# Kernel optimization log

Hardware: AMD Instinct MI355X
Metric: run time of the kernel (lower is better)

The kernel has to match this reference:

```python
import jax, jax.numpy as jnp
import numpy as np

N, H, IN, E = 4096, 64, 64, 10  # notes, hidden, input feat, edge types


def setup_inputs() -> dict:
    key = jax.random.key(0)
    ks = jax.random.split(key, 7)
    std_a = (2.0 / (H + H)) ** 0.5
    std_b = (2.0 / (IN + H)) ** 0.5
    return {
        "input": jax.random.normal(ks[0], (1, N, IN), jnp.float32),
        "hidden": jax.random.normal(ks[1], (1, N, H), jnp.float32),
        # dense per-edge-type adjacency; scaled by 1/N to keep gate pre-activations O(1)
        "edge_matrix": jax.random.uniform(ks[2], (E, N, N), jnp.float32) / N,
        "ba": jnp.zeros((H,), jnp.float32),
        "wz_wr_wh": jax.random.normal(ks[3], (E, H, 3 * H), jnp.float32) * std_a,
        "uz_ur": jax.random.normal(ks[4], (H, 2 * H), jnp.float32) * std_a,
        "uh": jax.random.normal(ks[5], (H, H), jnp.float32) * std_a,
        "input_wzrh": jax.random.normal(ks[6], (IN, 3 * H), jnp.float32) * std_b,
        "iteration": 10,
    }


def reference(input, hidden, edge_matrix, ba, wz_wr_wh, uz_ur, uh, input_wzrh, iteration):
    B, n, _ = input.shape          # B == 1
    h_dim = uh.shape[0]
    n_type = wz_wr_wh.shape[0]
    edge_T = jnp.swapaxes(edge_matrix, 1, 2)          # [E, N, N]
    inp_wzrh = jnp.matmul(input, input_wzrh)          # [B, N, 3H] (loop-invariant)

    def step(h, _):
        # message aggregation per edge type: [E,N,N] @ [B,N,H] -> [E,N,H]
        act = jnp.matmul(edge_T, h) + ba
        # per-edge-type gate projections: [E,N,H] @ [E,H,3H] -> [E,N,3H]
        act_wzrh = jnp.matmul(act, wz_wr_wh) + inp_wzrh
        wz, wr, wh = jnp.split(act_wzrh, 3, axis=-1)
        uz, ur = jnp.split(jnp.matmul(h, uz_ur), 2, axis=-1)  # [B,N,H] each
        z = jax.nn.sigmoid(wz.sum(0) + uz)
        r = jax.nn.sigmoid(wr.sum(0) + ur)
        h_tilde = jnp.tanh(wh.reshape(B, n_type, n, h_dim).sum(1)
                           + jnp.matmul(r * h, uh))
        return (1.0 - z) * h + z * h_tilde, None

    hidden, _ = jax.lax.scan(step, hidden, None, length=iteration)
    return hidden
```

## Files before the change

### kernel.cpp

```cpp
#include <hip/hip_runtime.h>
#include <hip/hip_bf16.h>


typedef __bf16 bf16;
typedef bf16 bf16x8 __attribute__((ext_vector_type(8)));
typedef float f32x4 __attribute__((ext_vector_type(4)));

static_assert(sizeof(bf16) == 2, "bf16 size");

constexpr int kN = 4096;
constexpr int kH = 64;
constexpr int kE = 10;
constexpr int kIter = 10;

constexpr size_t OFF_EDGET = 0;
constexpr size_t SZ_EDGET  = (size_t)kE * kN * kN * 2;
constexpr size_t OFF_HF32  = OFF_EDGET + SZ_EDGET;
constexpr size_t OFF_HBF   = OFF_HF32 + (size_t)kN * kH * 4;
constexpr size_t OFF_HT    = OFF_HBF + (size_t)kN * kH * 2;
constexpr size_t OFF_S     = OFF_HT + (size_t)kN * kH * 2;
constexpr size_t OFF_SBIAS = OFF_S + (size_t)kN * 192 * 4;
constexpr size_t OFF_WT    = OFF_SBIAS + (size_t)kN * 192 * 4;
constexpr size_t OFF_UZT   = OFF_WT + (size_t)kE * 192 * 64 * 2;
constexpr size_t OFF_UHT   = OFF_UZT + (size_t)128 * 64 * 2;
constexpr size_t WS_NEEDED = OFF_UHT + (size_t)64 * 64 * 2;

__device__ __forceinline__ void async16(const void* g, void* l) {
  __builtin_amdgcn_global_load_lds(
      (const __attribute__((address_space(1))) unsigned int*)g,
      (__attribute__((address_space(3))) unsigned int*)l, 16, 0, 0);
}

__device__ __forceinline__ float sigmoidf_(float x) { return 1.0f / (1.0f + __expf(-x)); }
__device__ __forceinline__ float tanhf_(float x) { return 1.0f - 2.0f / (__expf(2.0f * x) + 1.0f); }


__global__ __launch_bounds__(256) void k_transpose(const float* __restrict__ edge,
                                                   bf16* __restrict__ edgeT) {
  const int e = blockIdx.z;
  const int m0 = blockIdx.y * 64;
  const int n0 = blockIdx.x * 64;
  __shared__ bf16 t[64 * 66];
  const float* src = edge + (size_t)e * kN * kN;
  for (int i = threadIdx.x; i < 4096; i += 256) {
    int m = i >> 6, n = i & 63;
    t[n * 66 + m] = (bf16)src[(size_t)(m0 + m) * kN + n0 + n];
  }
  __syncthreads();
  bf16* dst = edgeT + (size_t)e * kN * kN;
  for (int i = threadIdx.x; i < 4096; i += 256) {
    int n = i >> 6, m = i & 63;
    dst[(size_t)(n0 + n) * kN + m0 + m] = t[n * 66 + m];
  }
}

__global__ __launch_bounds__(256) void k_weights(const float* __restrict__ wzwrwh,
                                                 const float* __restrict__ uz_ur,
                                                 const float* __restrict__ uh,
                                                 bf16* __restrict__ WT_all,
                                                 bf16* __restrict__ uzurT,
                                                 bf16* __restrict__ uhT) {
  int idx = blockIdx.x * 256 + threadIdx.x;
  if (idx < kE * 192 * 64) {
    int e = idx / (192 * 64);
    int rem = idx % (192 * 64);
    int c = rem / 64, hh = rem % 64;
    WT_all[idx] = (bf16)wzwrwh[((size_t)e * 64 + hh) * 192 + c];
  }
  if (idx < 128 * 64) {
    int c = idx / 64, hh = idx % 64;
    uzurT[idx] = (bf16)uz_ur[hh * 128 + c];
  }
  if (idx < 64 * 64) {
    int c = idx / 64, hh = idx % 64;
    uhT[idx] = (bf16)uh[hh * 64 + c];
  }
}

__global__ __launch_bounds__(256) void k_hinit(const float* __restrict__ hidden,
                                               float* __restrict__ hf32,
                                               bf16* __restrict__ hbf,
                                               bf16* __restrict__ hT) {
  int idx = blockIdx.x * 256 + threadIdx.x;
  float x = hidden[idx];
  hf32[idx] = x;
  hbf[idx] = (bf16)x;
  int n = idx >> 6, c = idx & 63;
  hT[(size_t)c * kN + n] = (bf16)x;
}

__global__ __launch_bounds__(256) void k_sbias(const float* __restrict__ input,
                                               const float* __restrict__ input_wzrh,
                                               float* __restrict__ SBias,
                                               float* __restrict__ S) {
  int idx = blockIdx.x * 256 + threadIdx.x;
  int n = idx / 192, c = idx % 192;
  float a = 0.f;
#pragma unroll 8
  for (int k = 0; k < 64; k++) a += input[n * 64 + k] * input_wzrh[k * 192 + c];
  a *= (float)kE;
  SBias[idx] = a;
  S[idx] = a;
}

__global__ __launch_bounds__(256) void k_copy(const float* __restrict__ src, float* __restrict__ dst) {
  int idx = blockIdx.x * 256 + threadIdx.x;
  dst[idx] = src[idx];
}

__global__ __launch_bounds__(256, 3) void kA(const bf16* __restrict__ edgeT,
                                             const bf16* __restrict__ hT,
                                             const bf16* __restrict__ WT_all,
                                             const float* __restrict__ ba,
                                             float* __restrict__ S) {
  const int e = blockIdx.y;
  const int n0 = blockIdx.x * 64;
  const int tid = threadIdx.x;
  const int lane = tid & 63;
  const int w = tid >> 6;
  const int l15 = lane & 15;
  const int q = lane >> 4;

  __shared__ bf16 Alds[64 * 64];
  __shared__ bf16 Blds[64 * 64];
  __shared__ bf16 Wlds[192 * 72];
  __shared__ bf16 actlds[64 * 72];

  {
    const bf16* src = WT_all + (size_t)e * 192 * 64;
    for (int i = tid; i < 192 * 8; i += 256) {
      int row = i >> 3, col = (i & 7) * 8;
      *(int4*)(Wlds + row * 72 + col) = *(const int4*)(src + row * 64 + col);
    }
  }

  f32x4 acc[4] = {};
  const bf16* Abase = edgeT + (size_t)e * kN * kN + (size_t)n0 * kN;

  for (int k0 = 0; k0 < kN; k0 += 64) {
    __syncthreads();
#pragma unroll
    for (int i = 0; i < 2; i++) {
      int c = i * 256 + tid;
      int row = c >> 3;
      int col = ((c & 7) ^ (row & 7)) * 8;
      async16(Abase + (size_t)row * kN + k0 + col, Alds + c * 8);
    }
#pragma unroll
    for (int i = 0; i < 2; i++) {
      int c = i * 256 + tid;
      int row = c >> 3;
      int col = ((c & 7) ^ (row & 7)) * 8;
      async16(hT + (size_t)row * kN + k0 + col, Blds + c * 8);
    }
    __syncthreads();
#pragma unroll
    for (int ks = 0; ks < 2; ks++) {
      const int ar = w * 16 + l15;
      bf16x8 af = *(const bf16x8*)(Alds + ar * 64 + ((ks * 32 + q * 8) ^ ((ar & 7) << 3)));
#pragma unroll
      for (int ct = 0; ct < 4; ct++) {
        const int br = ct * 16 + l15;
        bf16x8 bf = *(const bf16x8*)(Blds + br * 64 + ((ks * 32 + q * 8) ^ ((br & 7) << 3)));
        acc[ct] = __builtin_amdgcn_mfma_f32_16x16x32_bf16(af, bf, acc[ct], 0, 0, 0);
      }
    }
  }

  __syncthreads();
#pragma unroll
  for (int ct = 0; ct < 4; ct++) {
    int col = ct * 16 + l15;
    float bav = ba[col];
#pragma unroll
    for (int r = 0; r < 4; r++) {
      int row = w * 16 + q * 4 + r;
      actlds[row * 72 + col] = (bf16)(acc[ct][r] + bav);
    }
  }
  __syncthreads();

  f32x4 acc2[12] = {};
#pragma unroll
  for (int ks = 0; ks < 2; ks++) {
    bf16x8 af = *(const bf16x8*)(actlds + (w * 16 + l15) * 72 + ks * 32 + q * 8);
#pragma unroll
    for (int ct = 0; ct < 12; ct++) {
      bf16x8 bf = *(const bf16x8*)(Wlds + (ct * 16 + l15) * 72 + ks * 32 + q * 8);
      acc2[ct] = __builtin_amdgcn_mfma_f32_16x16x32_bf16(af, bf, acc2[ct], 0, 0, 0);
    }
  }
#pragma unroll
  for (int ct = 0; ct < 12; ct++) {
    int col = ct * 16 + l15;
#pragma unroll
    for (int r = 0; r < 4; r++) {
      int row = n0 + w * 16 + q * 4 + r;
      unsafeAtomicAdd(&S[(size_t)row * 192 + col], acc2[ct][r]);
    }
  }
}

__global__ __launch_bounds__(256) void kB(float* __restrict__ S,
                                          const float* __restrict__ SBias,
                                          const bf16* __restrict__ hbf,
                                          const float* __restrict__ hf32,
                                          const bf16* __restrict__ uzurT,
                                          const bf16* __restrict__ uhT,
                                          float* __restrict__ hf32_out,
                                          bf16* __restrict__ hbf_out,
                                          bf16* __restrict__ hT_out,
                                          float* __restrict__ dst) {
  const int n0 = blockIdx.x * 64;
  const int tid = threadIdx.x;
  const int lane = tid & 63;
  const int w = tid >> 6;
  const int l15 = lane & 15;
  const int q = lane >> 4;

  __shared__ bf16 hA[64 * 72];
  __shared__ bf16 uzT[128 * 72];
  __shared__ bf16 uhl[64 * 72];
  __shared__ bf16 rhl[64 * 72];

  for (int i = tid; i < 64 * 8; i += 256) {
    int row = i >> 3, col = (i & 7) * 8;
    *(int4*)(hA + row * 72 + col) = *(const int4*)(hbf + (size_t)(n0 + row) * 64 + col);
  }
  for (int i = tid; i < 128 * 8; i += 256) {
    int row = i >> 3, col = (i & 7) * 8;
    *(int4*)(uzT + row * 72 + col) = *(const int4*)(uzurT + (size_t)row * 64 + col);
  }
  for (int i = tid; i < 64 * 8; i += 256) {
    int row = i >> 3, col = (i & 7) * 8;
    *(int4*)(uhl + row * 72 + col) = *(const int4*)(uhT + (size_t)row * 64 + col);
  }
  __syncthreads();

  f32x4 u[8] = {};
#pragma unroll
  for (int ks = 0; ks < 2; ks++) {
    bf16x8 af = *(const bf16x8*)(hA + (w * 16 + l15) * 72 + ks * 32 + q * 8);
#pragma unroll
    for (int ct = 0; ct < 8; ct++) {
      bf16x8 bf = *(const bf16x8*)(uzT + (ct * 16 + l15) * 72 + ks * 32 + q * 8);
      u[ct] = __builtin_amdgcn_mfma_f32_16x16x32_bf16(af, bf, u[ct], 0, 0, 0);
    }
  }

  float zv[4][4], hv[4][4];
#pragma unroll
  for (int ct = 0; ct < 4; ct++) {
    int col = ct * 16 + l15;
#pragma unroll
    for (int r = 0; r < 4; r++) {
      int row = n0 + w * 16 + q * 4 + r;
      float sz = S[(size_t)row * 192 + col];
      float sr = S[(size_t)row * 192 + 64 + col];
      float z = sigmoidf_(sz + u[ct][r]);
      float rr = sigmoidf_(sr + u[4 + ct][r]);
      float h = hf32[(size_t)row * 64 + col];
      zv[ct][r] = z;
      hv[ct][r] = h;
      rhl[(w * 16 + q * 4 + r) * 72 + col] = (bf16)(rr * h);
    }
  }
  __syncthreads();

  f32x4 t[4] = {};
#pragma unroll
  for (int ks = 0; ks < 2; ks++) {
    bf16x8 af = *(const bf16x8*)(rhl + (w * 16 + l15) * 72 + ks * 32 + q * 8);
#pragma unroll
    for (int ct = 0; ct < 4; ct++) {
      bf16x8 bf = *(const bf16x8*)(uhl + (ct * 16 + l15) * 72 + ks * 32 + q * 8);
      t[ct] = __builtin_amdgcn_mfma_f32_16x16x32_bf16(af, bf, t[ct], 0, 0, 0);
    }
  }

  float hn[4][4];
#pragma unroll
  for (int ct = 0; ct < 4; ct++) {
    int col = ct * 16 + l15;
#pragma unroll
    for (int r = 0; r < 4; r++) {
      int row = n0 + w * 16 + q * 4 + r;
      float wh = S[(size_t)row * 192 + 128 + col];
      float htl = tanhf_(wh + t[ct][r]);
      float z = zv[ct][r];
      float v = (1.0f - z) * hv[ct][r] + z * htl;
      hn[ct][r] = v;
      dst[(size_t)row * 64 + col] = v;
      if (dst != hf32_out) hf32_out[(size_t)row * 64 + col] = v;
      hbf_out[(size_t)row * 64 + col] = (bf16)v;
    }
  }
  __syncthreads();

#pragma unroll
  for (int ct = 0; ct < 4; ct++) {
#pragma unroll
    for (int r = 0; r < 4; r++) {
      int row = w * 16 + q * 4 + r, col = ct * 16 + l15;
      rhl[row * 72 + col] = (bf16)hn[ct][r];
    }
  }
  for (int i = tid; i < 64 * 192; i += 256) S[(size_t)n0 * 192 + i] = SBias[(size_t)n0 * 192 + i];
  __syncthreads();
  for (int i = tid; i < 4096; i += 256) {
    int c = i >> 6, n = i & 63;
    hT_out[(size_t)c * kN + n0 + n] = rhl[n * 72 + c];
  }
}

extern "C" void kernel_launch(void* const* d_in, const int* in_sizes, int n_in,
                              void* d_out, int out_size, void* d_ws, size_t ws_size,
                              hipStream_t stream) {
  const float* input = (const float*)d_in[0];
  const float* hidden = (const float*)d_in[1];
  const float* edge = (const float*)d_in[2];
  const float* ba = (const float*)d_in[3];
  const float* wzwrwh = (const float*)d_in[4];
  const float* uz_ur = (const float*)d_in[5];
  const float* uh = (const float*)d_in[6];
  const float* input_wzrh = (const float*)d_in[7];
  float* out = (float*)d_out;

  if (ws_size < WS_NEEDED) {
    k_copy<<<kN * kH / 256, 256, 0, stream>>>(hidden, out);
    return;
  }

  char* ws = (char*)d_ws;
  bf16* edgeT = (bf16*)(ws + OFF_EDGET);
  float* hf32 = (float*)(ws + OFF_HF32);
  bf16* hbf = (bf16*)(ws + OFF_HBF);
  bf16* hT = (bf16*)(ws + OFF_HT);
  float* S = (float*)(ws + OFF_S);
  float* SBias = (float*)(ws + OFF_SBIAS);
  bf16* WT_all = (bf16*)(ws + OFF_WT);
  bf16* uzurT = (bf16*)(ws + OFF_UZT);
  bf16* uhT = (bf16*)(ws + OFF_UHT);

  k_transpose<<<dim3(kN / 64, kN / 64, kE), 256, 0, stream>>>(edge, edgeT);
  k_weights<<<(kE * 192 * 64) / 256, 256, 0, stream>>>(wzwrwh, uz_ur, uh, WT_all, uzurT, uhT);
  k_hinit<<<(kN * kH) / 256, 256, 0, stream>>>(hidden, hf32, hbf, hT);
  k_sbias<<<(kN * 192) / 256, 256, 0, stream>>>(input, input_wzrh, SBias, S);

  for (int it = 0; it < kIter; it++) {
    kA<<<dim3(kN / 64, kE), 256, 0, stream>>>(edgeT, hT, WT_all, ba, S);
    float* dst = (it == kIter - 1) ? out : hf32;
    kB<<<kN / 64, 256, 0, stream>>>(S, SBias, hbf, hf32, uzurT, uhT, hf32, hbf, hT, dst);
  }
}
```

Before: 2.144 ms.

## Replace atomic accumulation of gate sums with per-edge-type partial buffers reduced in kB

kA now writes its per-edge-type gate projections into a separate partial buffer for each edge type with plain stores, instead of atomically adding into one shared S buffer. kB sums the ten partials plus the bias into LDS before the gate math, and no longer has to reset S for the next iteration. kA also reads the weight B-fragments straight from global memory instead of staging them in LDS, which frees LDS, and the occupancy hint is dropped from its launch bounds. The cost is ten times more intermediate memory traffic (about 31 MB written and read per iteration) plus a larger LDS footprint in kB.

```diff
diff --git a/kernel.cpp b/kernel.cpp
--- a/kernel.cpp
+++ b/kernel.cpp
@@ -18,8 +18,8 @@
 constexpr size_t OFF_HF32  = OFF_EDGET + SZ_EDGET;
 constexpr size_t OFF_HBF   = OFF_HF32 + (size_t)kN * kH * 4;
 constexpr size_t OFF_HT    = OFF_HBF + (size_t)kN * kH * 2;
-constexpr size_t OFF_S     = OFF_HT + (size_t)kN * kH * 2;
-constexpr size_t OFF_SBIAS = OFF_S + (size_t)kN * 192 * 4;
+constexpr size_t OFF_SPART = OFF_HT + (size_t)kN * kH * 2;
+constexpr size_t OFF_SBIAS = OFF_SPART + (size_t)kE * kN * 192 * 4;
 constexpr size_t OFF_WT    = OFF_SBIAS + (size_t)kN * 192 * 4;
 constexpr size_t OFF_UZT   = OFF_WT + (size_t)kE * 192 * 64 * 2;
 constexpr size_t OFF_UHT   = OFF_UZT + (size_t)128 * 64 * 2;
@@ -91,16 +91,13 @@
 
 __global__ __launch_bounds__(256) void k_sbias(const float* __restrict__ input,
                                                const float* __restrict__ input_wzrh,
-                                               float* __restrict__ SBias,
-                                               float* __restrict__ S) {
+                                               float* __restrict__ SBias) {
   int idx = blockIdx.x * 256 + threadIdx.x;
   int n = idx / 192, c = idx % 192;
   float a = 0.f;
 #pragma unroll 8
   for (int k = 0; k < 64; k++) a += input[n * 64 + k] * input_wzrh[k * 192 + c];
-  a *= (float)kE;
-  SBias[idx] = a;
-  S[idx] = a;
+  SBias[idx] = a * (float)kE;
 }
 
 __global__ __launch_bounds__(256) void k_copy(const float* __restrict__ src, float* __restrict__ dst) {
@@ -108,11 +105,11 @@
   dst[idx] = src[idx];
 }
 
-__global__ __launch_bounds__(256, 3) void kA(const bf16* __restrict__ edgeT,
-                                             const bf16* __restrict__ hT,
-                                             const bf16* __restrict__ WT_all,
-                                             const float* __restrict__ ba,
-                                             float* __restrict__ S) {
+__global__ __launch_bounds__(256) void kA(const bf16* __restrict__ edgeT,
+                                          const bf16* __restrict__ hT,
+                                          const bf16* __restrict__ WT_all,
+                                          const float* __restrict__ ba,
+                                          float* __restrict__ Spart) {
   const int e = blockIdx.y;
   const int n0 = blockIdx.x * 64;
   const int tid = threadIdx.x;
@@ -123,16 +120,7 @@
 
   __shared__ bf16 Alds[64 * 64];
   __shared__ bf16 Blds[64 * 64];
-  __shared__ bf16 Wlds[192 * 72];
   __shared__ bf16 actlds[64 * 72];
-
-  {
-    const bf16* src = WT_all + (size_t)e * 192 * 64;
-    for (int i = tid; i < 192 * 8; i += 256) {
-      int row = i >> 3, col = (i & 7) * 8;
-      *(int4*)(Wlds + row * 72 + col) = *(const int4*)(src + row * 64 + col);
-    }
-  }
 
   f32x4 acc[4] = {};
   const bf16* Abase = edgeT + (size_t)e * kN * kN + (size_t)n0 * kN;
@@ -180,28 +168,31 @@
   }
   __syncthreads();
 
+  const bf16* Wg = WT_all + (size_t)e * 192 * 64;
   f32x4 acc2[12] = {};
 #pragma unroll
   for (int ks = 0; ks < 2; ks++) {
     bf16x8 af = *(const bf16x8*)(actlds + (w * 16 + l15) * 72 + ks * 32 + q * 8);
 #pragma unroll
     for (int ct = 0; ct < 12; ct++) {
-      bf16x8 bf = *(const bf16x8*)(Wlds + (ct * 16 + l15) * 72 + ks * 32 + q * 8);
+      bf16x8 bf = *(const bf16x8*)(Wg + (ct * 16 + l15) * 64 + ks * 32 + q * 8);
       acc2[ct] = __builtin_amdgcn_mfma_f32_16x16x32_bf16(af, bf, acc2[ct], 0, 0, 0);
     }
   }
+
+  float* Sp = Spart + (size_t)e * kN * 192;
 #pragma unroll
   for (int ct = 0; ct < 12; ct++) {
     int col = ct * 16 + l15;
 #pragma unroll
     for (int r = 0; r < 4; r++) {
       int row = n0 + w * 16 + q * 4 + r;
-      unsafeAtomicAdd(&S[(size_t)row * 192 + col], acc2[ct][r]);
-    }
-  }
-}
-
-__global__ __launch_bounds__(256) void kB(float* __restrict__ S,
+      Sp[(size_t)row * 192 + col] = acc2[ct][r];
+    }
+  }
+}
+
+__global__ __launch_bounds__(256) void kB(const float* __restrict__ Spart,
                                           const float* __restrict__ SBias,
                                           const bf16* __restrict__ hbf,
                                           const float* __restrict__ hf32,
@@ -218,6 +209,7 @@
   const int l15 = lane & 15;
   const int q = lane >> 4;
 
+  __shared__ float Slds[64 * 193];
   __shared__ bf16 hA[64 * 72];
   __shared__ bf16 uzT[128 * 72];
   __shared__ bf16 uhl[64 * 72];
@@ -235,6 +227,15 @@
     int row = i >> 3, col = (i & 7) * 8;
     *(int4*)(uhl + row * 72 + col) = *(const int4*)(uhT + (size_t)row * 64 + col);
   }
+
+  for (int i = tid; i < 64 * 192; i += 256) {
+    int row = i / 192, col = i % 192;
+    size_t g = (size_t)(n0 + row) * 192 + col;
+    float s = SBias[g];
+#pragma unroll
+    for (int e = 0; e < kE; e++) s += Spart[(size_t)e * kN * 192 + g];
+    Slds[row * 193 + col] = s;
+  }
   __syncthreads();
 
   f32x4 u[8] = {};
@@ -254,15 +255,16 @@
     int col = ct * 16 + l15;
 #pragma unroll
     for (int r = 0; r < 4; r++) {
-      int row = n0 + w * 16 + q * 4 + r;
-      float sz = S[(size_t)row * 192 + col];
-      float sr = S[(size_t)row * 192 + 64 + col];
+      int lrow = w * 16 + q * 4 + r;
+      int row = n0 + lrow;
+      float sz = Slds[lrow * 193 + col];
+      float sr = Slds[lrow * 193 + 64 + col];
       float z = sigmoidf_(sz + u[ct][r]);
       float rr = sigmoidf_(sr + u[4 + ct][r]);
       float h = hf32[(size_t)row * 64 + col];
       zv[ct][r] = z;
       hv[ct][r] = h;
-      rhl[(w * 16 + q * 4 + r) * 72 + col] = (bf16)(rr * h);
+      rhl[lrow * 72 + col] = (bf16)(rr * h);
     }
   }
   __syncthreads();
@@ -284,8 +286,9 @@
     int col = ct * 16 + l15;
 #pragma unroll
     for (int r = 0; r < 4; r++) {
-      int row = n0 + w * 16 + q * 4 + r;
-      float wh = S[(size_t)row * 192 + 128 + col];
+      int lrow = w * 16 + q * 4 + r;
+      int row = n0 + lrow;
+      float wh = Slds[lrow * 193 + 128 + col];
       float htl = tanhf_(wh + t[ct][r]);
       float z = zv[ct][r];
       float v = (1.0f - z) * hv[ct][r] + z * htl;
@@ -305,7 +308,6 @@
       rhl[row * 72 + col] = (bf16)hn[ct][r];
     }
   }
-  for (int i = tid; i < 64 * 192; i += 256) S[(size_t)n0 * 192 + i] = SBias[(size_t)n0 * 192 + i];
   __syncthreads();
   for (int i = tid; i < 4096; i += 256) {
     int c = i >> 6, n = i & 63;
@@ -336,7 +338,7 @@
   float* hf32 = (float*)(ws + OFF_HF32);
   bf16* hbf = (bf16*)(ws + OFF_HBF);
   bf16* hT = (bf16*)(ws + OFF_HT);
-  float* S = (float*)(ws + OFF_S);
+  float* Spart = (float*)(ws + OFF_SPART);
   float* SBias = (float*)(ws + OFF_SBIAS);
   bf16* WT_all = (bf16*)(ws + OFF_WT);
   bf16* uzurT = (bf16*)(ws + OFF_UZT);
@@ -345,11 +347,12 @@
   k_transpose<<<dim3(kN / 64, kN / 64, kE), 256, 0, stream>>>(edge, edgeT);
   k_weights<<<(kE * 192 * 64) / 256, 256, 0, stream>>>(wzwrwh, uz_ur, uh, WT_all, uzurT, uhT);
   k_hinit<<<(kN * kH) / 256, 256, 0, stream>>>(hidden, hf32, hbf, hT);
-  k_sbias<<<(kN * 192) / 256, 256, 0, stream>>>(input, input_wzrh, SBias, S);
+  k_sbias<<<(kN * 192) / 256, 256, 0, stream>>>(input, input_wzrh, SBias);
 
   for (int it = 0; it < kIter; it++) {
-    kA<<<dim3(kN / 64, kE), 256, 0, stream>>>(edgeT, hT, WT_all, ba, S);
+    kA<<<dim3(kN / 64, kE), 256, 0, stream>>>(edgeT, hT, WT_all, ba, Spart);
     float* dst = (it == kIter - 1) ? out : hf32;
-    kB<<<kN / 64, 256, 0, stream>>>(S, SBias, hbf, hf32, uzurT, uhT, hf32, hbf, hT, dst);
-  }
-}
+    kB<<<kN / 64, 256, 0, stream>>>(Spart, SBias, hbf, hf32, uzurT, uhT,
+                                    hf32, hbf, hT, dst);
+  }
+}
```

New measurement: 2.130 ms. No clear change (-0.7%).
